# Kernel optimization log

Measured on AMD Instinct MI355X. Metric: run time of the kernel, lower is better.

## Reference

```python
import jax, jax.numpy as jnp
import numpy as np
import math

N_HEADS = 16
ROPE_BASE = 10000.0


def rotate_half(x):
    x1 = x[..., ::2]
    x2 = x[..., 1::2]
    return jnp.stack((-x2, x1), axis=-1).reshape(x.shape)


def rope_tables(seq_len, head_dim, dtype):
    inv_freq = 1.0 / (ROPE_BASE ** (jnp.arange(0, head_dim, 2, dtype=jnp.float32) / head_dim))
    positions = jnp.arange(seq_len, dtype=jnp.float32)
    freqs = jnp.outer(positions, inv_freq)            # [S, hd/2]
    emb = jnp.concatenate((freqs, freqs), axis=-1)    # [S, hd]  (matches torch cat convention)
    cos = jnp.cos(emb)[None, None, :, :].astype(dtype)
    sin = jnp.sin(emb)[None, None, :, :].astype(dtype)
    return cos, sin


def setup_inputs() -> dict:
    key = jax.random.key(0)
    k1, k2, k3 = jax.random.split(key, 3)
    B, S, D = 2, 2048, 1024
    x = jax.random.normal(k1, (B, S, D), dtype=jnp.float32)
    # causal lower-triangular mask, broadcastable over batch and heads
    mask = jnp.tril(jnp.ones((S, S), dtype=jnp.int32))[None, None, :, :]
    w_qkv = jax.random.normal(k2, (D, 3 * D), dtype=jnp.float32) * 0.02
    w_out = jax.random.normal(k3, (D, D), dtype=jnp.float32) * 0.02
    return {"x": x, "mask": mask, "w_qkv": w_qkv, "w_out": w_out}


def reference(x, mask, w_qkv, w_out):
    B, S, D = x.shape
    H = N_HEADS
    hd = D // H
    qkv = (x @ w_qkv).reshape(B, S, 3, H, hd)
    qkv = jnp.transpose(qkv, (2, 0, 3, 1, 4))         # [3, B, H, S, hd]
    q, k, v = qkv[0], qkv[1], qkv[2]
    cos, sin = rope_tables(S, hd, x.dtype)
    q = q * cos + rotate_half(q) * sin
    k = k * cos + rotate_half(k) * sin
    scale = math.sqrt(hd)
    attn = jnp.einsum("bhsd,bhtd->bhst", q, k) / scale
    attn = jnp.where(mask == 0, -jnp.inf, attn)
    attn = jax.nn.softmax(attn, axis=-1)              # dropout p=0.0 -> identity
    out = jnp.einsum("bhst,bhtd->bhsd", attn, v)
    out = jnp.transpose(out, (0, 2, 1, 3)).reshape(B, S, D)
    return out @ w_out
```

## Files before the change

### kernel.cpp

```cpp
#include <hip/hip_runtime.h>
#include <stdint.h>

typedef unsigned short u16;
typedef __bf16 bf16x8 __attribute__((ext_vector_type(8)));
typedef float f32x4 __attribute__((ext_vector_type(4)));

#define S_LEN 2048
#define NH    16
#define DM    1024
#define N3    3072
#define MROWS 4096

__device__ __forceinline__ float b2f(u16 u) {
  unsigned int v = ((unsigned int)u) << 16;
  return __builtin_bit_cast(float, v);
}
__device__ __forceinline__ u16 f2b(float f) {
  unsigned int v = __builtin_bit_cast(unsigned int, f);
  v += 0x7fffu + ((v >> 16) & 1u);
  return (u16)(v >> 16);
}
__device__ __forceinline__ u16 f2b_trunc(float f) {
  return (u16)(__builtin_bit_cast(unsigned int, f) >> 16);
}
__device__ __forceinline__ bf16x8 ld8(const u16* p) { return *(const bf16x8*)p; }
__device__ __forceinline__ f32x4 mfma16(bf16x8 a, bf16x8 b, f32x4 c) {
  return __builtin_amdgcn_mfma_f32_16x16x32_bf16(a, b, c, 0, 0, 0);
}
__device__ __forceinline__ void glds16(const void* g, void* l) {
  __builtin_amdgcn_global_load_lds(
      (const __attribute__((address_space(1))) unsigned int*)g,
      (__attribute__((address_space(3))) unsigned int*)l, 16, 0, 0);
}
__device__ __forceinline__ int bfish(unsigned int w) {
  unsigned int e = (w >> 7) & 0xffu;
  return (e >= 100u && e <= 134u) ? 1 : 0;
}

__global__ __launch_bounds__(256) void prep_kernel(const void* __restrict__ x,
                                                   const void* __restrict__ wqkv,
                                                   const void* __restrict__ wout,
                                                   u16* __restrict__ xb,
                                                   u16* __restrict__ wqT,
                                                   u16* __restrict__ woT,
                                                   float* __restrict__ cosT,
                                                   float* __restrict__ sinT,
                                                   int* __restrict__ flag) {
  const int bx = blockIdx.x;
  const int t = threadIdx.x;
  if (bx < 2048) {
    __shared__ int cnt;
    if (t == 0) cnt = 0;
    __syncthreads();
    size_t i = (size_t)bx * 256 + t;
    const uint4* xv = (const uint4*)x;
    uint4 probe = xv[i];
    unsigned int wds[4]; *(uint4*)wds = probe;
    atomicAdd(&cnt, bfish(wds[0]) + bfish(wds[1]) + bfish(wds[2]) + bfish(wds[3]));
    __syncthreads();
    const int isbf = cnt > 512;
    if (t == 0) *flag = isbf;
    if (isbf) {
      ((uint4*)xb)[i] = probe;
    } else {
      const float* xf = (const float*)x;
      #pragma unroll
      for (int j = 0; j < 8; ++j) xb[i * 8 + j] = f2b(xf[i * 8 + j]);
    }
    return;
  }
  if (bx < 2304) {
    int i = (bx - 2048) * 256 + t;
    int s = i >> 5, f = i & 31;
    float invf = expf(-(float)(2 * f) * (1.0f / 64.0f) * logf(10000.0f));
    float th = (float)s * invf;
    float sv, cv;
    sincosf(th, &sv, &cv);
    cosT[s * 64 + f] = cv; cosT[s * 64 + 32 + f] = cv;
    sinT[s * 64 + f] = sv; sinT[s * 64 + 32 + f] = sv;
    return;
  }
  const int wq = bx < 5376;
  const int id = wq ? (bx - 2304) : (bx - 5376);
  const int ncx = wq ? 96 : 32;
  const void* in = wq ? wqkv : wout;
  u16* out = wq ? wqT : woT;
  const int C = wq ? 3072 : 1024;
  const int bxc = id % ncx, byr = id / ncx;
  __shared__ int cnt;
  __shared__ float tile[32][33];
  const int tx = t & 31, ty = t >> 5;
  if (t == 0) cnt = 0;
  __syncthreads();
  const unsigned int* wv = (const unsigned int*)in;
  size_t off = (((size_t)id) * 256 + t) & 524287;
  atomicAdd(&cnt, bfish(wv[off]));
  __syncthreads();
  const int fl = cnt > 128;
  const int c0 = bxc * 32, r0 = byr * 32;
  #pragma unroll
  for (int dy = 0; dy < 32; dy += 8) {
    size_t idx = (size_t)(r0 + ty + dy) * C + (c0 + tx);
    float v = fl ? b2f(((const u16*)in)[idx]) : ((const float*)in)[idx];
    tile[ty + dy][tx] = v;
  }
  __syncthreads();
  #pragma unroll
  for (int dy = 0; dy < 32; dy += 8) {
    out[(size_t)(c0 + ty + dy) * 1024 + (r0 + tx)] = f2b(tile[tx][ty + dy]);
  }
}

__global__ __launch_bounds__(256) void gemm_qkv(const u16* __restrict__ A,
                                                const u16* __restrict__ Bt,
                                                u16* __restrict__ Qo,
                                                u16* __restrict__ Ko,
                                                u16* __restrict__ Vt,
                                                const float* __restrict__ cosT,
                                                const float* __restrict__ sinT) {
  __shared__ u16 smem[8192];
  u16* Al = smem;
  u16* Bl = smem + 4096;
  const int t = threadIdx.x;
  const int lane = t & 63, wave = t >> 6;
  const int ln = lane & 15, quad = lane >> 4;
  const int wr = wave >> 1, wc = wave & 1;
  const int m0 = blockIdx.x * 128, n0 = blockIdx.y * 128;
  const int rr = t >> 2;
  const int cb = (t & 3) * 16;
  const char* Ab = (const char*)A;
  const char* Bb = (const char*)Bt;
  f32x4 acc[4][4] = {};

  for (int k0 = 0; k0 < 1024; k0 += 32) {
    __syncthreads();
    glds16(Ab + ((size_t)(m0 + rr) * 1024 + k0) * 2 + cb,      (char*)Al + t * 16);
    glds16(Ab + ((size_t)(m0 + 64 + rr) * 1024 + k0) * 2 + cb, (char*)Al + 4096 + t * 16);
    glds16(Bb + ((size_t)(n0 + rr) * 1024 + k0) * 2 + cb,      (char*)Bl + t * 16);
    glds16(Bb + ((size_t)(n0 + 64 + rr) * 1024 + k0) * 2 + cb, (char*)Bl + 4096 + t * 16);
    __syncthreads();
    bf16x8 a[4], b[4];
    #pragma unroll
    for (int i = 0; i < 4; ++i) a[i] = ld8(Al + (wr * 64 + i * 16 + ln) * 32 + quad * 8);
    #pragma unroll
    for (int j = 0; j < 4; ++j) b[j] = ld8(Bl + (wc * 64 + j * 16 + ln) * 32 + quad * 8);
    #pragma unroll
    for (int i = 0; i < 4; ++i)
      #pragma unroll
      for (int j = 0; j < 4; ++j)
        acc[i][j] = mfma16(a[i], b[j], acc[i][j]);
  }

  const int which = n0 >> 10;
  if (which < 2) {
    u16* dst = which ? Ko : Qo;
    const float qs = which ? 1.0f : 0.18033688011112042f;
    #pragma unroll
    for (int i = 0; i < 4; ++i)
      #pragma unroll
      for (int j = 0; j < 4; ++j) {
        const int c = n0 + wc * 64 + j * 16 + ln;
        const int h = (c >> 6) & 15, d = c & 63;
        const float sgn = (d & 1) ? 1.0f : -1.0f;
        #pragma unroll
        for (int r = 0; r < 4; ++r) {
          const int m = m0 + wr * 64 + i * 16 + quad * 4 + r;
          const int s = m & 2047, b_ = m >> 11;
          const float v = acc[i][j][r];
          const float p = __shfl_xor(v, 1);
          const float o = (v * cosT[s * 64 + d] + sgn * p * sinT[s * 64 + d]) * qs;
          dst[((size_t)(b_ * NH + h) * S_LEN + s) * 64 + d] = f2b(o);
        }
      }
  } else {
    #pragma unroll
    for (int i = 0; i < 4; ++i)
      #pragma unroll
      for (int j = 0; j < 4; ++j) {
        const int c = n0 + wc * 64 + j * 16 + ln;
        const int h = (c >> 6) & 15, d = c & 63;
        const int m = m0 + wr * 64 + i * 16 + quad * 4;
        const int s = m & 2047, b_ = m >> 11;
        u16 pk[4];
        #pragma unroll
        for (int r = 0; r < 4; ++r) pk[r] = f2b(acc[i][j][r]);
        *(uint2*)&Vt[((size_t)(b_ * NH + h) * 64 + d) * S_LEN + s] = *(const uint2*)pk;
      }
  }
}

__global__ __launch_bounds__(256) void attn_kernel(const u16* __restrict__ Qb,
                                                   const u16* __restrict__ Kb,
                                                   const u16* __restrict__ Vt,
                                                   u16* __restrict__ Ao) {
  __shared__ u16 smem[20480];
  u16* Kl = smem;
  u16* Vl = smem + 8192;
  u16* Pl = smem + 16384;
  const int t = threadIdx.x;
  const int lane = t & 63, w = t >> 6;
  const int ln = lane & 15, quad = lane >> 4;
  const int i = blockIdx.x;
  const int xcd = i & 7;
  const int j = i >> 3;
  const int bh = (xcd << 2) | (j & 3);
  const int q5 = j >> 2;
  const int g = q5 & 7, s5 = q5 >> 3;
  const int qt = (s5 & 1) ? (31 - ((s5 >> 1) << 3) - g) : (((s5 >> 1) << 3) + g);
  const int q0 = qt * 64;
  const int b = bh >> 4, h = bh & 15;
  const u16* Qbh = Qb + (size_t)bh * (S_LEN * 64);
  const u16* Kbh = Kb + (size_t)bh * (S_LEN * 64);
  const u16* Vtbh = Vt + (size_t)bh * (64 * S_LEN);
  u16* Plw = Pl + w * 1024;
  u16* AoBase = Ao + (size_t)b * S_LEN * DM + h * 64;

  auto stage = [&](int kt, int bufi) {
    u16* kd = Kl + bufi * 4096;
    u16* vd = Vl + bufi * 4096;
    const u16* kg = Kbh + (size_t)kt * 64 * 64;
    const u16* vg = Vtbh + (size_t)kt * 64;
    #pragma unroll
    for (int it = 0; it < 2; ++it) {
      int c = it * 256 + t;
      int row = c >> 3, sg = (c & 7) ^ (row & 7);
      glds16((const char*)kg + ((size_t)row * 64 + sg * 8) * 2,   (char*)kd + c * 16);
      glds16((const char*)vg + ((size_t)row * 2048 + sg * 8) * 2, (char*)vd + c * 16);
    }
  };

  bf16x8 aq[2];
  #pragma unroll
  for (int kk = 0; kk < 2; ++kk)
    aq[kk] = ld8(Qbh + (size_t)(q0 + w * 16 + ln) * 64 + kk * 32 + quad * 8);

  f32x4 o[4] = {};
  float l[4] = {0.f, 0.f, 0.f, 0.f};

  stage(0, 0);
  __syncthreads();

  for (int kt = 0; kt <= qt; ++kt) {
    const int bufi = kt & 1;
    if (kt < qt) stage(kt + 1, bufi ^ 1);
    const u16* Kb_ = Kl + bufi * 4096;
    const u16* Vb_ = Vl + bufi * 4096;

    f32x4 sc[4] = {};
    #pragma unroll
    for (int kk = 0; kk < 2; ++kk)
      #pragma unroll
      for (int ct = 0; ct < 4; ++ct) {
        bf16x8 bk = ld8(Kb_ + (ct * 16 + ln) * 64 + (((kk * 4 + quad) ^ (ln & 7)) << 3));
        sc[ct] = mfma16(aq[kk], bk, sc[ct]);
      }

    if (kt == qt) {
      #pragma unroll
      for (int ct = 0; ct < 4; ++ct)
        #pragma unroll
        for (int r = 0; r < 4; ++r) {
          const int row = quad * 4 + r;
          float p = ((ct * 16 + ln) > (w * 16 + row))
                        ? 0.f : __builtin_amdgcn_exp2f(sc[ct][r]);
          l[r] += p;
          Plw[row * 64 + ((((ct * 2) + (ln >> 3)) ^ quad) << 3) + (ln & 7)] = f2b_trunc(p);
        }
    } else {
      #pragma unroll
      for (int ct = 0; ct < 4; ++ct)
        #pragma unroll
        for (int r = 0; r < 4; ++r) {
          const int row = quad * 4 + r;
          float p = __builtin_amdgcn_exp2f(sc[ct][r]);
          l[r] += p;
          Plw[row * 64 + ((((ct * 2) + (ln >> 3)) ^ quad) << 3) + (ln & 7)] = f2b_trunc(p);
        }
    }

    #pragma unroll
    for (int k4 = 0; k4 < 2; ++k4) {
      bf16x8 ap = ld8(Plw + ln * 64 + (((k4 * 4 + quad) ^ (ln >> 2)) << 3));
      #pragma unroll
      for (int dt = 0; dt < 4; ++dt) {
        bf16x8 bv = ld8(Vb_ + (dt * 16 + ln) * 64 + (((k4 * 4 + quad) ^ (ln & 7)) << 3));
        o[dt] = mfma16(ap, bv, o[dt]);
      }
    }
    __syncthreads();
  }

  #pragma unroll
  for (int r = 0; r < 4; ++r) {
    float lv = l[r];
    #pragma unroll
    for (int off = 1; off < 16; off <<= 1) lv += __shfl_xor(lv, off);
    l[r] = 1.f / lv;
  }
  #pragma unroll
  for (int dt = 0; dt < 4; ++dt)
    #pragma unroll
    for (int r = 0; r < 4; ++r) {
      float v = o[dt][r] * l[r];
      AoBase[(size_t)(q0 + w * 16 + quad * 4 + r) * DM + dt * 16 + ln] = f2b(v);
    }
}

template <int TM>
__global__ __launch_bounds__(256) void gemm_out_t(const u16* __restrict__ A,
                                                  const u16* __restrict__ Bt,
                                                  void* __restrict__ Out,
                                                  const int* __restrict__ flag) {
  constexpr int MI = TM / 32;
  __shared__ u16 smem[(TM + 128) * 32];
  u16* Al = smem;
  u16* Bl = smem + TM * 32;
  const int t = threadIdx.x;
  const int lane = t & 63, wave = t >> 6;
  const int ln = lane & 15, quad = lane >> 4;
  const int wr = wave >> 1, wc = wave & 1;
  const int m0 = blockIdx.x * TM, n0 = blockIdx.y * 128;
  const int rr = t >> 2;
  const int cb = (t & 3) * 16;
  const char* Ab = (const char*)A;
  const char* Bb = (const char*)Bt;
  f32x4 acc[MI][4] = {};

  for (int k0 = 0; k0 < 1024; k0 += 32) {
    __syncthreads();
    #pragma unroll
    for (int p = 0; p < TM / 64; ++p)
      glds16(Ab + ((size_t)(m0 + p * 64 + rr) * 1024 + k0) * 2 + cb,
             (char*)Al + p * 4096 + t * 16);
    glds16(Bb + ((size_t)(n0 + rr) * 1024 + k0) * 2 + cb,      (char*)Bl + t * 16);
    glds16(Bb + ((size_t)(n0 + 64 + rr) * 1024 + k0) * 2 + cb, (char*)Bl + 4096 + t * 16);
    __syncthreads();
    bf16x8 a[MI], b[4];
    #pragma unroll
    for (int i = 0; i < MI; ++i)
      a[i] = ld8(Al + (wr * (TM / 2) + i * 16 + ln) * 32 + quad * 8);
    #pragma unroll
    for (int j = 0; j < 4; ++j)
      b[j] = ld8(Bl + (wc * 64 + j * 16 + ln) * 32 + quad * 8);
    #pragma unroll
    for (int i = 0; i < MI; ++i)
      #pragma unroll
      for (int j = 0; j < 4; ++j)
        acc[i][j] = mfma16(a[i], b[j], acc[i][j]);
  }

  const int fl = *flag;
  #pragma unroll
  for (int i = 0; i < MI; ++i)
    #pragma unroll
    for (int j = 0; j < 4; ++j)
      #pragma unroll
      for (int r = 0; r < 4; ++r) {
        int m = m0 + wr * (TM / 2) + i * 16 + quad * 4 + r;
        int c = n0 + wc * 64 + j * 16 + ln;
        float v = acc[i][j][r];
        if (fl) ((u16*)Out)[(size_t)m * DM + c] = f2b(v);
        else    ((float*)Out)[(size_t)m * DM + c] = v;
      }
}

extern "C" void kernel_launch(void* const* d_in, const int* in_sizes, int n_in,
                              void* d_out, int out_size, void* d_ws, size_t ws_size,
                              hipStream_t stream) {
  (void)in_sizes; (void)n_in; (void)out_size; (void)ws_size;
  const void* x    = d_in[0];
  const void* wqkv = d_in[2];
  const void* wout = d_in[3];
  char* ws = (char*)d_ws;
  u16*  xb   = (u16*)(ws + 0);
  u16*  Ao   = xb;
  u16*  wqT  = (u16*)(ws + 8388608);
  u16*  woT  = (u16*)(ws + 14680064);
  u16*  Qb   = (u16*)(ws + 16777216);
  u16*  Kb   = (u16*)(ws + 25165824);
  u16*  Vt   = (u16*)(ws + 33554432);
  float* cosT = (float*)(ws + 41943040);
  float* sinT = (float*)(ws + 42467328);
  int*  flag = (int*)(ws + 42991616);

  prep_kernel<<<6400, 256, 0, stream>>>(x, wqkv, wout, xb, wqT, woT, cosT, sinT, flag);
  gemm_qkv<<<dim3(32, 24), 256, 0, stream>>>(xb, wqT, Qb, Kb, Vt, cosT, sinT);
  attn_kernel<<<1024, 256, 0, stream>>>(Qb, Kb, Vt, Ao);
  gemm_out_t<64><<<dim3(64, 8), 256, 0, stream>>>(Ao, woT, d_out, flag);
}
```

Baseline: 203.2 us.

## Deepen QKV GEMM K-tile with swizzled LDS and transpose attention MFMA operands

The QKV projection GEMM now stages 64-wide K slices per iteration into a doubled LDS buffer with an XOR swizzle. This halves the number of barrier pairs and aims to reduce LDS bank conflicts. The attention kernel swaps MFMA operand order so scores and outputs come out transposed: each lane owns one query row, and P writes and output stores become packed 8-byte vector stores. The row-sum reduction shrinks to two shuffles. The larger LDS footprint may reduce occupancy of the GEMM.

After: 193.8 us. 4.6% less time.

```diff
diff --git a/kernel.cpp b/kernel.cpp
--- a/kernel.cpp
+++ b/kernel.cpp
@@ -118,37 +118,51 @@
                                                 u16* __restrict__ Vt,
                                                 const float* __restrict__ cosT,
                                                 const float* __restrict__ sinT) {
-  __shared__ u16 smem[8192];
+  __shared__ u16 smem[16384];
   u16* Al = smem;
-  u16* Bl = smem + 4096;
+  u16* Bl = smem + 8192;
   const int t = threadIdx.x;
   const int lane = t & 63, wave = t >> 6;
   const int ln = lane & 15, quad = lane >> 4;
   const int wr = wave >> 1, wc = wave & 1;
   const int m0 = blockIdx.x * 128, n0 = blockIdx.y * 128;
-  const int rr = t >> 2;
-  const int cb = (t & 3) * 16;
   const char* Ab = (const char*)A;
   const char* Bb = (const char*)Bt;
   f32x4 acc[4][4] = {};
 
-  for (int k0 = 0; k0 < 1024; k0 += 32) {
-    __syncthreads();
-    glds16(Ab + ((size_t)(m0 + rr) * 1024 + k0) * 2 + cb,      (char*)Al + t * 16);
-    glds16(Ab + ((size_t)(m0 + 64 + rr) * 1024 + k0) * 2 + cb, (char*)Al + 4096 + t * 16);
-    glds16(Bb + ((size_t)(n0 + rr) * 1024 + k0) * 2 + cb,      (char*)Bl + t * 16);
-    glds16(Bb + ((size_t)(n0 + 64 + rr) * 1024 + k0) * 2 + cb, (char*)Bl + 4096 + t * 16);
-    __syncthreads();
-    bf16x8 a[4], b[4];
-    #pragma unroll
-    for (int i = 0; i < 4; ++i) a[i] = ld8(Al + (wr * 64 + i * 16 + ln) * 32 + quad * 8);
-    #pragma unroll
-    for (int j = 0; j < 4; ++j) b[j] = ld8(Bl + (wc * 64 + j * 16 + ln) * 32 + quad * 8);
+  for (int k0 = 0; k0 < 1024; k0 += 64) {
+    __syncthreads();
+    #pragma unroll
+    for (int it = 0; it < 4; ++it) {
+      int c = it * 256 + t;
+      int row = c >> 3;
+      int sg = (c & 7) ^ (row & 7);
+      glds16(Ab + ((size_t)(m0 + row) * 1024 + k0 + sg * 8) * 2, (char*)Al + c * 16);
+      glds16(Bb + ((size_t)(n0 + row) * 1024 + k0 + sg * 8) * 2, (char*)Bl + c * 16);
+    }
+    __syncthreads();
+    bf16x8 a[4][2], b[4][2];
+    #pragma unroll
+    for (int i = 0; i < 4; ++i) {
+      const int row = wr * 64 + i * 16 + ln;
+      #pragma unroll
+      for (int ki = 0; ki < 2; ++ki)
+        a[i][ki] = ld8(Al + row * 64 + (((ki * 4 + quad) ^ (row & 7)) << 3));
+    }
+    #pragma unroll
+    for (int j = 0; j < 4; ++j) {
+      const int row = wc * 64 + j * 16 + ln;
+      #pragma unroll
+      for (int ki = 0; ki < 2; ++ki)
+        b[j][ki] = ld8(Bl + row * 64 + (((ki * 4 + quad) ^ (row & 7)) << 3));
+    }
     #pragma unroll
     for (int i = 0; i < 4; ++i)
       #pragma unroll
-      for (int j = 0; j < 4; ++j)
-        acc[i][j] = mfma16(a[i], b[j], acc[i][j]);
+      for (int j = 0; j < 4; ++j) {
+        acc[i][j] = mfma16(a[i][0], b[j][0], acc[i][j]);
+        acc[i][j] = mfma16(a[i][1], b[j][1], acc[i][j]);
+      }
   }
 
   const int which = n0 >> 10;
@@ -229,13 +243,13 @@
     }
   };
 
-  bf16x8 aq[2];
+  bf16x8 bq[2];
   #pragma unroll
   for (int kk = 0; kk < 2; ++kk)
-    aq[kk] = ld8(Qbh + (size_t)(q0 + w * 16 + ln) * 64 + kk * 32 + quad * 8);
+    bq[kk] = ld8(Qbh + (size_t)(q0 + w * 16 + ln) * 64 + kk * 32 + quad * 8);
 
   f32x4 o[4] = {};
-  float l[4] = {0.f, 0.f, 0.f, 0.f};
+  float l = 0.f;
 
   stage(0, 0);
   __syncthreads();
@@ -246,64 +260,54 @@
     const u16* Kb_ = Kl + bufi * 4096;
     const u16* Vb_ = Vl + bufi * 4096;
 
-    f32x4 sc[4] = {};
+    f32x4 st[4] = {};
     #pragma unroll
     for (int kk = 0; kk < 2; ++kk)
       #pragma unroll
       for (int ct = 0; ct < 4; ++ct) {
-        bf16x8 bk = ld8(Kb_ + (ct * 16 + ln) * 64 + (((kk * 4 + quad) ^ (ln & 7)) << 3));
-        sc[ct] = mfma16(aq[kk], bk, sc[ct]);
-      }
-
-    if (kt == qt) {
-      #pragma unroll
-      for (int ct = 0; ct < 4; ++ct)
-        #pragma unroll
-        for (int r = 0; r < 4; ++r) {
-          const int row = quad * 4 + r;
-          float p = ((ct * 16 + ln) > (w * 16 + row))
-                        ? 0.f : __builtin_amdgcn_exp2f(sc[ct][r]);
-          l[r] += p;
-          Plw[row * 64 + ((((ct * 2) + (ln >> 3)) ^ quad) << 3) + (ln & 7)] = f2b_trunc(p);
-        }
-    } else {
-      #pragma unroll
-      for (int ct = 0; ct < 4; ++ct)
-        #pragma unroll
-        for (int r = 0; r < 4; ++r) {
-          const int row = quad * 4 + r;
-          float p = __builtin_amdgcn_exp2f(sc[ct][r]);
-          l[r] += p;
-          Plw[row * 64 + ((((ct * 2) + (ln >> 3)) ^ quad) << 3) + (ln & 7)] = f2b_trunc(p);
-        }
+        bf16x8 ak = ld8(Kb_ + (ct * 16 + ln) * 64 + (((kk * 4 + quad) ^ (ln & 7)) << 3));
+        st[ct] = mfma16(ak, bq[kk], st[ct]);
+      }
+
+    const bool diag = (kt == qt);
+    #pragma unroll
+    for (int ct = 0; ct < 4; ++ct) {
+      u16 pk[4];
+      #pragma unroll
+      for (int r = 0; r < 4; ++r) {
+        float p;
+        if (diag && (ct * 16 + quad * 4 + r) > (w * 16 + ln)) p = 0.f;
+        else p = __builtin_amdgcn_exp2f(st[ct][r]);
+        l += p;
+        pk[r] = f2b_trunc(p);
+      }
+      *(uint2*)(Plw + ln * 64 + ((((ct * 2) + (quad >> 1)) ^ (ln & 7)) << 3)
+                + ((quad & 1) << 2)) = *(const uint2*)pk;
     }
 
     #pragma unroll
     for (int k4 = 0; k4 < 2; ++k4) {
-      bf16x8 ap = ld8(Plw + ln * 64 + (((k4 * 4 + quad) ^ (ln >> 2)) << 3));
+      bf16x8 bp = ld8(Plw + ln * 64 + (((k4 * 4 + quad) ^ (ln & 7)) << 3));
       #pragma unroll
       for (int dt = 0; dt < 4; ++dt) {
-        bf16x8 bv = ld8(Vb_ + (dt * 16 + ln) * 64 + (((k4 * 4 + quad) ^ (ln & 7)) << 3));
-        o[dt] = mfma16(ap, bv, o[dt]);
-      }
-    }
-    __syncthreads();
-  }
-
-  #pragma unroll
-  for (int r = 0; r < 4; ++r) {
-    float lv = l[r];
-    #pragma unroll
-    for (int off = 1; off < 16; off <<= 1) lv += __shfl_xor(lv, off);
-    l[r] = 1.f / lv;
-  }
-  #pragma unroll
-  for (int dt = 0; dt < 4; ++dt)
-    #pragma unroll
-    for (int r = 0; r < 4; ++r) {
-      float v = o[dt][r] * l[r];
-      AoBase[(size_t)(q0 + w * 16 + quad * 4 + r) * DM + dt * 16 + ln] = f2b(v);
-    }
+        bf16x8 av = ld8(Vb_ + (dt * 16 + ln) * 64 + (((k4 * 4 + quad) ^ (ln & 7)) << 3));
+        o[dt] = mfma16(av, bp, o[dt]);
+      }
+    }
+    __syncthreads();
+  }
+
+  l += __shfl_xor(l, 16);
+  l += __shfl_xor(l, 32);
+  const float inv = 1.f / l;
+  const size_t qrow = (size_t)(q0 + w * 16 + ln) * DM;
+  #pragma unroll
+  for (int dt = 0; dt < 4; ++dt) {
+    u16 pk[4];
+    #pragma unroll
+    for (int r = 0; r < 4; ++r) pk[r] = f2b(o[dt][r] * inv);
+    *(uint2*)(AoBase + qrow + dt * 16 + quad * 4) = *(const uint2*)pk;
+  }
 }
 
 template <int TM>
```
